# Kernel tuning notes

Measured on AMD Instinct MI355X. Metric: run time of the kernel, lower is better.

Reference implementation:

```python
import jax, jax.numpy as jnp
import numpy as np
from jax import lax

DIM = 1024
HEADS = 16
KERNEL = 7
STRIDE = 4
EPS = 1e-5


def setup_inputs() -> dict:
    key = jax.random.key(0)
    ks = jax.random.split(key, 4)
    B, N = 2, 4096
    w_scale = 0.02
    return {
        "x": jax.random.normal(ks[0], (B, N, DIM), dtype=jnp.float32),
        "ln_w": jnp.ones((DIM,), jnp.float32),
        "ln_b": jnp.zeros((DIM,), jnp.float32),
        "Wk": jax.random.normal(ks[1], (DIM, DIM, KERNEL), dtype=jnp.float32) * w_scale,
        "Wv": jax.random.normal(ks[2], (DIM, DIM, KERNEL), dtype=jnp.float32) * w_scale,
        "Wq": jax.random.normal(ks[3], (DIM, DIM, KERNEL), dtype=jnp.float32) * w_scale,
    }


def _conv1d(x_bnd, w):
    # x: (B, N, D) -> conv over sequence dim with 'same' padding; w: (out_ch, in_ch, K)
    x_cn = jnp.transpose(x_bnd, (0, 2, 1))  # (B, D, N)
    pad = KERNEL // 2
    y = lax.conv_general_dilated(
        x_cn, w, window_strides=(1,), padding=[(pad, pad)],
        dimension_numbers=("NCH", "OIH", "NCH"))
    return jnp.transpose(y, (0, 2, 1))  # (B, N, D)


def reference(x, ln_w, ln_b, Wk, Wv, Wq):
    B, N, D = x.shape
    hd = D // HEADS
    # LayerNorm (biased variance, as in torch)
    mu = jnp.mean(x, axis=-1, keepdims=True)
    var = jnp.mean(jnp.square(x - mu), axis=-1, keepdims=True)
    x_n = (x - mu) / jnp.sqrt(var + EPS) * ln_w + ln_b

    K = _conv1d(x_n, Wk)                 # (B, N, D)
    V = _conv1d(x_n, Wv)                 # (B, N, D)
    Q = _conv1d(x_n, Wq)[:, ::STRIDE]    # (B, M, D) windowed queries
    M = Q.shape[1]

    Qh = Q.reshape(B, M, HEADS, hd).transpose(0, 2, 1, 3)  # (B, H, M, hd)
    Kh = K.reshape(B, N, HEADS, hd).transpose(0, 2, 1, 3)  # (B, H, N, hd)
    Vh = V.reshape(B, N, HEADS, hd).transpose(0, 2, 1, 3)  # (B, H, N, hd)

    scale = jnp.sqrt(jnp.asarray(hd, x.dtype))
    scores = jnp.einsum("bhmd,bhnd->bhmn", Qh, Kh) / scale  # (B, H, M, N)
    attn = jax.nn.softmax(scores, axis=-1)
    out = jnp.einsum("bhmn,bhnd->bhmd", attn, Vh)           # (B, H, M, hd)
    out = out.transpose(0, 2, 1, 3).reshape(B, M, D)
    return out + Q
```

## Files before the change

kernel.cpp:

```cpp
#include <hip/hip_runtime.h>

typedef __attribute__((ext_vector_type(4))) float f32x4;
typedef __attribute__((ext_vector_type(16))) float f32x16;
typedef __attribute__((ext_vector_type(8))) short short8;
typedef __attribute__((ext_vector_type(4))) unsigned short u16x4;
typedef __attribute__((ext_vector_type(8))) unsigned short u16x8;

#define AS1 __attribute__((address_space(1)))
#define AS3 __attribute__((address_space(3)))

__device__ __forceinline__ unsigned short f2bf(float f) {
  unsigned u = __float_as_uint(f);
  return (unsigned short)((u + 0x7FFFu + ((u >> 16) & 1u)) >> 16);
}
__device__ __forceinline__ unsigned short f2bf_fast(float f) {
  return (unsigned short)((__float_as_uint(f) + 0x8000u) >> 16);
}

__global__ __launch_bounds__(256) void ln_kernel(
    const float* __restrict__ x, const float* __restrict__ lw,
    const float* __restrict__ lb, unsigned short* __restrict__ xpad) {
  __shared__ float red[8];
  int row = blockIdx.x;
  int b = row >> 12, n = row & 4095;
  const float* xr = x + (size_t)row * 1024;
  int c = threadIdx.x * 4;
  f32x4 v = *(const f32x4*)(xr + c);
  float s = v[0] + v[1] + v[2] + v[3];
  float sq = v[0]*v[0] + v[1]*v[1] + v[2]*v[2] + v[3]*v[3];
#pragma unroll
  for (int off = 32; off; off >>= 1) {
    s  += __shfl_xor(s, off, 64);
    sq += __shfl_xor(sq, off, 64);
  }
  int w = threadIdx.x >> 6;
  if ((threadIdx.x & 63) == 0) { red[w*2] = s; red[w*2+1] = sq; }
  __syncthreads();
  float S  = red[0]+red[2]+red[4]+red[6];
  float SQ = red[1]+red[3]+red[5]+red[7];
  float mean = S * (1.0f/1024.0f);
  float var  = SQ * (1.0f/1024.0f) - mean*mean;
  float rstd = rsqrtf(var + 1e-5f);
  f32x4 wv = *(const f32x4*)(lw + c);
  f32x4 bv = *(const f32x4*)(lb + c);
  u16x4 o;
#pragma unroll
  for (int r = 0; r < 4; ++r) o[r] = f2bf((v[r]-mean)*rstd*wv[r] + bv[r]);
  *(u16x4*)(xpad + (((size_t)(b*4102 + n + 3)) << 10) + c) = o;
}

__global__ __launch_bounds__(256) void repack_kernel(
    const float* __restrict__ Wk, const float* __restrict__ Wv,
    const float* __restrict__ Wq, unsigned short* __restrict__ Wt) {
  __shared__ unsigned short t[7168];
  const float* W = (blockIdx.y == 0) ? Wk : (blockIdx.y == 1) ? Wv : Wq;
  int o = blockIdx.x;
  const float* row = W + (size_t)o * 7168;
  unsigned short* orow = Wt + ((size_t)(blockIdx.y * 1024 + o)) * 7168;
#pragma unroll
  for (int p = 0; p < 7; ++p) {
    int idx = p*1024 + threadIdx.x*4;
    f32x4 v = *(const f32x4*)(row + idx);
#pragma unroll
    for (int e = 0; e < 4; ++e) {
      unsigned j = idx + e;
      unsigned i = (j * 149797u) >> 20;
      unsigned k = j - i*7;
      t[k*1024 + i] = f2bf(v[e]);
    }
  }
  __syncthreads();
#pragma unroll
  for (int p = 0; p < 7; ++p) {
    int idx = p*1024 + threadIdx.x*4;
    *(u16x4*)(orow + idx) = *(const u16x4*)(t + idx);
  }
}

__global__ __launch_bounds__(256, 4) void conv3(
    const unsigned short* __restrict__ Apad,
    const unsigned short* __restrict__ Wt,
    unsigned short* __restrict__ Ksg, unsigned short* __restrict__ Vsg,
    unsigned short* __restrict__ Qsg, float* __restrict__ Qf) {
  __shared__ unsigned short As[128*64];
  __shared__ unsigned short Bs[128*64];
  const int g = blockIdx.x;
  const int tid = threadIdx.x;
  const int w = tid >> 6, l = tid & 63;

  int mode, nt, rt;
  if (g < 1024) {
    int xcol = ((g & 7) << 1) | ((g >> 3) & 1);
    mode = (xcol < 8) ? 0 : 1;
    nt = xcol; rt = g >> 4;
  } else {
    int gq = g - 1024;
    mode = 2; nt = 16 + (gq & 7); rt = gq >> 3;
  }
  const int n0 = nt << 7;
  const int r0 = rt << 7;

  const int lrow = l >> 3;
  const int cs = (l & 7) ^ lrow;
  size_t abase0, astep, bbase0;
  {
    int r = r0 + (w << 5) + lrow;
    int bb, nn;
    if (mode == 2) { bb = r >> 10; nn = (r & 1023) << 2; astep = 8 * 4096; }
    else           { bb = r >> 12; nn = r & 4095;        astep = 8 * 1024; }
    abase0 = (((size_t)(bb*4102 + nn)) << 10) + cs*8;
    int nc = n0 + (w << 5) + lrow;
    bbase0 = (size_t)nc * 7168 + cs*8;
  }

  f32x16 acc[2][2] = {};
  const int wm = (w >> 1) << 6, wn = (w & 1) << 6;
  const int l31 = l & 31, lh = l >> 5, l7 = l & 7;

  for (int k0 = 0; k0 < 7168; k0 += 64) {
    __syncthreads();
#pragma unroll
    for (int t = 0; t < 4; ++t) {
      __builtin_amdgcn_global_load_lds((const AS1 void*)(Apad + abase0 + (size_t)t*astep + k0),
                                       (AS3 void*)(As + (((w << 2) + t) << 9)), 16, 0, 0);
      __builtin_amdgcn_global_load_lds((const AS1 void*)(Wt + bbase0 + (size_t)t*(8*7168) + k0),
                                       (AS3 void*)(Bs + (((w << 2) + t) << 9)), 16, 0, 0);
    }
    __syncthreads();
#pragma unroll
    for (int s2 = 0; s2 < 2; ++s2) {
      short8 af[2][2], bf[2][2];
#pragma unroll
      for (int i = 0; i < 2; ++i)
#pragma unroll
        for (int hs = 0; hs < 2; ++hs) {
          int s = (s2 << 1) | hs;
          int ch = (((s << 1) | lh) ^ l7) << 3;
          af[i][hs] = *(const short8*)(As + (wm + (i<<5) + l31)*64 + ch);
          bf[i][hs] = *(const short8*)(Bs + (wn + (i<<5) + l31)*64 + ch);
        }
#pragma unroll
      for (int hs = 0; hs < 2; ++hs)
#pragma unroll
        for (int i = 0; i < 2; ++i)
#pragma unroll
          for (int j = 0; j < 2; ++j)
            acc[i][j] = __builtin_amdgcn_mfma_f32_32x32x16_bf16(af[i][hs], bf[j][hs], acc[i][j], 0, 0, 0);
    }
  }

  if (mode == 0) {
#pragma unroll
    for (int i = 0; i < 2; ++i) {
      int rgb = r0 + wm + (i<<5);
      int b = rgb >> 12, nbase = rgb & 4095;
#pragma unroll
      for (int j = 0; j < 2; ++j) {
        int cg = n0 + wn + (j<<5) + l31;
        int h = cg >> 6, kd = (cg >> 5) & 1;
        size_t base = ((size_t)(((b*16 + h)*2 + kd)) << 12) * 32 + (size_t)(cg & 31);
#pragma unroll
        for (int r = 0; r < 16; ++r) {
          int nb = nbase + (r & 3) + ((r >> 2) << 3) + (lh << 2);
          Ksg[base + ((size_t)nb << 5)] = f2bf(acc[i][j][r]);
        }
      }
    }
  } else if (mode == 1) {
#pragma unroll
    for (int i = 0; i < 2; ++i) {
      int rgb = r0 + wm + (i<<5);
      int b = rgb >> 12, nbase = rgb & 4095;
      int nc = nbase >> 5;
#pragma unroll
      for (int j = 0; j < 2; ++j) {
        int c = n0 + wn + (j<<5) + l31 - 1024;
        int h = c >> 6, d = c & 63;
        size_t rowbase = ((size_t)((b*16 + h)*128 + nc) * 64 + d) << 5;
#pragma unroll
        for (int g2 = 0; g2 < 4; ++g2) {
          u16x4 pv;
#pragma unroll
          for (int e = 0; e < 4; ++e) pv[e] = f2bf(acc[i][j][g2*4 + e]);
          *(u16x4*)(Vsg + rowbase + (g2 << 3) + (lh << 2)) = pv;
        }
      }
    }
  } else {
#pragma unroll
    for (int i = 0; i < 2; ++i) {
      int rqb = r0 + wm + (i<<5);
#pragma unroll
      for (int j = 0; j < 2; ++j) {
        int cg = (n0 - 2048) + wn + (j<<5) + l31;
        int h = cg >> 6, kd = (cg >> 5) & 1, d32 = cg & 31;
#pragma unroll
        for (int r = 0; r < 16; ++r) {
          int rq = rqb + (r & 3) + ((r >> 2) << 3) + (lh << 2);
          int b = rq >> 10, m = rq & 1023;
          float vv = acc[i][j][r];
          Qsg[(((size_t)((b*16 + h)*2 + kd) * 1024 + m) << 5) + d32] = f2bf(vv);
          Qf[((size_t)rq << 10) + cg] = vv;
        }
      }
    }
  }
}

__global__ __launch_bounds__(256) void attn_kernel(
    const unsigned short* __restrict__ Ksg, const unsigned short* __restrict__ Vsg,
    const unsigned short* __restrict__ Qsg, const float* __restrict__ Qf,
    float* __restrict__ out) {
  __shared__ unsigned short Ks[8192];
  __shared__ unsigned short Vs[8192];
  __shared__ unsigned short Qs[4096];
  __shared__ unsigned short Ps[8704];
  const int tid = threadIdx.x, w = tid >> 6, l = tid & 63;
  const int g = blockIdx.x;
  const int bh = (g & 7) + (((g >> 3) & 3) << 3);
  const int qt = g >> 5;
  const int b = bh >> 4, h = bh & 15;
  const int m0 = qt << 6;
  const int quad = l >> 4, lc = l & 15, l3 = l & 3;
  const float C = 0.18033688011112042f;
  const int lsw = (l & 60) | ((l ^ (l >> 2)) & 3);

  const unsigned short* KgT = Ksg + ((size_t)bh << 18);
  const unsigned short* VgT = Vsg + ((size_t)bh << 18);
  const unsigned short* QgT = Qsg + ((size_t)bh << 16);

#pragma unroll
  for (int p = 0; p < 2; ++p) {
    int t = w*2 + p;
    int kd = t >> 2, ml = (t & 3) << 4;
    __builtin_amdgcn_global_load_lds(
        (const AS1 void*)(QgT + ((size_t)((kd << 10) + m0 + ml) << 5) + lsw*8),
        (AS3 void*)(Qs + (t << 9)), 16, 0, 0);
  }

  float l_run = 0.f;
  f32x4 oacc[4] = {};
  unsigned short* Pw = Ps + w*2176;

  for (int it = 0; it < 32; ++it) {
    int n0 = it << 7;
    __syncthreads();
#pragma unroll
    for (int p = 0; p < 4; ++p) {
      int t = (w << 2) + p;
      __builtin_amdgcn_global_load_lds(
          (const AS1 void*)(KgT + ((size_t)(((t >> 3) << 12) + n0 + ((t & 7) << 4)) << 5) + lsw*8),
          (AS3 void*)(Ks + (t << 9)), 16, 0, 0);
      __builtin_amdgcn_global_load_lds(
          (const AS1 void*)(VgT + ((size_t)((((n0 >> 5) + (t >> 2)) << 6) + ((t & 3) << 4)) << 5) + lsw*8),
          (AS3 void*)(Vs + (t << 9)), 16, 0, 0);
    }
    __syncthreads();

    const int ch = (quad ^ l3) << 3;
    short8 ak[8][2];
#pragma unroll
    for (int k = 0; k < 2; ++k)
#pragma unroll
      for (int ni = 0; ni < 8; ++ni)
        ak[ni][k] = *(const short8*)(Ks + (k << 12) + ((ni<<4) + lc)*32 + ch);

    f32x4 sv[8] = {};
#pragma unroll
    for (int k = 0; k < 2; ++k) {
      short8 bq = *(const short8*)(Qs + (k << 11) + ((w<<4) + lc)*32 + ch);
#pragma unroll
      for (int ni = 0; ni < 8; ++ni)
        sv[ni] = __builtin_amdgcn_mfma_f32_16x16x32_bf16(ak[ni][k], bq, sv[ni], 0, 0, 0);
    }

    float su = 0.f;
#pragma unroll
    for (int ni = 0; ni < 8; ++ni) {
      u16x4 pv;
#pragma unroll
      for (int rr = 0; rr < 4; ++rr) {
        float pp = __builtin_amdgcn_exp2f(sv[ni][rr] * C);
        su += pp;
        pv[rr] = f2bf_fast(pp);
      }
      *(u16x4*)(Pw + lc*136 + (ni<<4) + (quad<<2)) = pv;
    }
    su += __shfl_xor(su, 16, 64);
    su += __shfl_xor(su, 32, 64);
    l_run += su;

#pragma unroll
    for (int kn = 0; kn < 4; ++kn) {
      short8 bp = *(const short8*)(Pw + lc*136 + (kn<<5) + (quad<<3));
#pragma unroll
      for (int dt = 0; dt < 4; ++dt) {
        short8 av = *(const short8*)(Vs + (kn << 11) + ((dt<<4) + lc)*32 + ch);
        oacc[dt] = __builtin_amdgcn_mfma_f32_16x16x32_bf16(av, bp, oacc[dt], 0, 0, 0);
      }
    }
  }

  float invl = 1.0f / l_run;
  int m = m0 + (w<<4) + lc;
#pragma unroll
  for (int dt = 0; dt < 4; ++dt) {
    int d = (dt<<4) + (quad<<2);
    size_t off = (((size_t)(b << 10) + m) << 10) + (h << 6) + d;
    f32x4 qv = *(const f32x4*)(Qf + off);
    f32x4 ov;
#pragma unroll
    for (int rr = 0; rr < 4; ++rr) ov[rr] = oacc[dt][rr]*invl + qv[rr];
    *(f32x4*)(out + off) = ov;
  }
}

extern "C" void kernel_launch(void* const* d_in, const int* in_sizes, int n_in,
                              void* d_out, int out_size, void* d_ws, size_t ws_size,
                              hipStream_t stream) {
  const float* x  = (const float*)d_in[0];
  const float* lw = (const float*)d_in[1];
  const float* lb = (const float*)d_in[2];
  const float* Wk = (const float*)d_in[3];
  const float* Wv = (const float*)d_in[4];
  const float* Wq = (const float*)d_in[5];
  float* out = (float*)d_out;

  char* ws = (char*)d_ws;
  size_t off = 0;
  unsigned short* xpad = (unsigned short*)(ws + off); off += (size_t)2*4102*1024*2;
  unsigned short* Wt   = (unsigned short*)(ws + off); off += (size_t)3072*7168*2;
  unsigned short* Ksg  = (unsigned short*)(ws + off); off += (size_t)32*2*4096*32*2;
  unsigned short* Vsg  = (unsigned short*)(ws + off); off += (size_t)32*128*64*32*2;
  unsigned short* Qsg  = (unsigned short*)(ws + off); off += (size_t)32*2*1024*32*2;
  float*          Qf   = (float*)(ws + off);          off += (size_t)2048*1024*4;

  for (int b = 0; b < 2; ++b) {
    hipMemsetAsync(xpad + (size_t)b*4102*1024, 0, 3*1024*2, stream);
    hipMemsetAsync(xpad + ((size_t)b*4102 + 4099)*1024, 0, 3*1024*2, stream);
  }
  ln_kernel<<<dim3(8192), dim3(256), 0, stream>>>(x, lw, lb, xpad);
  repack_kernel<<<dim3(1024, 3), dim3(256), 0, stream>>>(Wk, Wv, Wq, Wt);
  conv3<<<dim3(1152), dim3(256), 0, stream>>>(xpad, Wt, Ksg, Vsg, Qsg, Qf);
  attn_kernel<<<dim3(512), dim3(256), 0, stream>>>(Ksg, Vsg, Qsg, Qf, out);
}
```

Measured before the change: 581.4 us.

## Rewrite conv GEMM as 256x256 double-buffered kernel with split-K Q tail

```diff
diff --git a/kernel.cpp b/kernel.cpp
--- a/kernel.cpp
+++ b/kernel.cpp
@@ -1,10 +1,8 @@
 #include <hip/hip_runtime.h>
 
 typedef __attribute__((ext_vector_type(4))) float f32x4;
-typedef __attribute__((ext_vector_type(16))) float f32x16;
 typedef __attribute__((ext_vector_type(8))) short short8;
 typedef __attribute__((ext_vector_type(4))) unsigned short u16x4;
-typedef __attribute__((ext_vector_type(8))) unsigned short u16x8;
 
 #define AS1 __attribute__((address_space(1)))
 #define AS3 __attribute__((address_space(3)))
@@ -77,134 +75,231 @@
   }
 }
 
-__global__ __launch_bounds__(256, 4) void conv3(
+__global__ __launch_bounds__(512, 2) void conv256(
     const unsigned short* __restrict__ Apad,
     const unsigned short* __restrict__ Wt,
     unsigned short* __restrict__ Ksg, unsigned short* __restrict__ Vsg,
-    unsigned short* __restrict__ Qsg, float* __restrict__ Qf) {
-  __shared__ unsigned short As[128*64];
-  __shared__ unsigned short Bs[128*64];
-  const int g = blockIdx.x;
+    float* __restrict__ Qf) {
+  __shared__ unsigned short As[2][2][8192];
+  __shared__ unsigned short Bs[2][2][8192];
+
   const int tid = threadIdx.x;
   const int w = tid >> 6, l = tid & 63;
-
-  int mode, nt, rt;
-  if (g < 1024) {
-    int xcol = ((g & 7) << 1) | ((g >> 3) & 1);
-    mode = (xcol < 8) ? 0 : 1;
-    nt = xcol; rt = g >> 4;
-  } else {
-    int gq = g - 1024;
-    mode = 2; nt = 16 + (gq & 7); rt = gq >> 3;
-  }
-  const int n0 = nt << 7;
-  const int r0 = rt << 7;
-
-  const int lrow = l >> 3;
-  const int cs = (l & 7) ^ lrow;
-  size_t abase0, astep, bbase0;
-  {
-    int r = r0 + (w << 5) + lrow;
-    int bb, nn;
-    if (mode == 2) { bb = r >> 10; nn = (r & 1023) << 2; astep = 8 * 4096; }
-    else           { bb = r >> 12; nn = r & 4095;        astep = 8 * 1024; }
-    abase0 = (((size_t)(bb*4102 + nn)) << 10) + cs*8;
-    int nc = n0 + (w << 5) + lrow;
-    bbase0 = (size_t)nc * 7168 + cs*8;
-  }
-
-  f32x16 acc[2][2] = {};
-  const int wm = (w >> 1) << 6, wn = (w & 1) << 6;
-  const int l31 = l & 31, lh = l >> 5, l7 = l & 7;
-
-  for (int k0 = 0; k0 < 7168; k0 += 64) {
-    __syncthreads();
-#pragma unroll
-    for (int t = 0; t < 4; ++t) {
-      __builtin_amdgcn_global_load_lds((const AS1 void*)(Apad + abase0 + (size_t)t*astep + k0),
-                                       (AS3 void*)(As + (((w << 2) + t) << 9)), 16, 0, 0);
-      __builtin_amdgcn_global_load_lds((const AS1 void*)(Wt + bbase0 + (size_t)t*(8*7168) + k0),
-                                       (AS3 void*)(Bs + (((w << 2) + t) << 9)), 16, 0, 0);
-    }
-    __syncthreads();
-#pragma unroll
-    for (int s2 = 0; s2 < 2; ++s2) {
-      short8 af[2][2], bf[2][2];
-#pragma unroll
-      for (int i = 0; i < 2; ++i)
-#pragma unroll
-        for (int hs = 0; hs < 2; ++hs) {
-          int s = (s2 << 1) | hs;
-          int ch = (((s << 1) | lh) ^ l7) << 3;
-          af[i][hs] = *(const short8*)(As + (wm + (i<<5) + l31)*64 + ch);
-          bf[i][hs] = *(const short8*)(Bs + (wn + (i<<5) + l31)*64 + ch);
-        }
-#pragma unroll
-      for (int hs = 0; hs < 2; ++hs)
-#pragma unroll
-        for (int i = 0; i < 2; ++i)
-#pragma unroll
-          for (int j = 0; j < 2; ++j)
-            acc[i][j] = __builtin_amdgcn_mfma_f32_32x32x16_bf16(af[i][hs], bf[j][hs], acc[i][j], 0, 0, 0);
-    }
-  }
-
-  if (mode == 0) {
-#pragma unroll
-    for (int i = 0; i < 2; ++i) {
-      int rgb = r0 + wm + (i<<5);
-      int b = rgb >> 12, nbase = rgb & 4095;
-#pragma unroll
-      for (int j = 0; j < 2; ++j) {
-        int cg = n0 + wn + (j<<5) + l31;
-        int h = cg >> 6, kd = (cg >> 5) & 1;
-        size_t base = ((size_t)(((b*16 + h)*2 + kd)) << 12) * 32 + (size_t)(cg & 31);
-#pragma unroll
-        for (int r = 0; r < 16; ++r) {
-          int nb = nbase + (r & 3) + ((r >> 2) << 3) + (lh << 2);
-          Ksg[base + ((size_t)nb << 5)] = f2bf(acc[i][j][r]);
+  const int wm = w >> 2, wn = w & 3;
+  const int l15 = l & 15, lh4 = l >> 4, l7 = l & 7;
+  const int chA = ((l7 & 4) | (lh4 ^ (l7 & 3))) << 3;
+  const int wOff = w << 9;
+  const int bid = blockIdx.x;
+  const int ct = bid & 7, rt = bid >> 3;
+
+  unsigned aOff[2][2], bOff[2][2];
+#pragma unroll
+  for (int i = 0; i < 2; ++i) {
+    const int idx = i * 512 + tid;
+    const int r = idx >> 3;
+    const int clog8 = (((idx & 7) ^ (r & 7)) << 3);
+#pragma unroll
+    for (int hh = 0; hh < 2; ++hh) {
+      const int rg = (rt << 8) + (hh << 7) + r;
+      aOff[hh][i] = ((unsigned)((rg >> 12) * 4102 + (rg & 4095)) << 10) + clog8;
+      const int cg = (ct << 8) + (hh << 7) + r;
+      bOff[hh][i] = (unsigned)cg * 7168u + clog8;
+    }
+  }
+
+  unsigned aRd[4], bRd[2];
+#pragma unroll
+  for (int fm = 0; fm < 4; ++fm)
+    aRd[fm] = (unsigned)(((wm << 6) + (fm << 4) + l15) << 6) + chA;
+#pragma unroll
+  for (int fn = 0; fn < 2; ++fn)
+    bRd[fn] = (unsigned)(((wn << 5) + (fn << 4) + l15) << 6) + chA;
+
+  f32x4 acc[2][2][4][2] = {};
+  short8 af[4][2], bfr[2][2];
+
+#define STGA(BUF, HALF, T) do { \
+    __builtin_amdgcn_global_load_lds((const AS1 void*)(Apad + aOff[HALF][0] + ((unsigned)(T) << 6)), (AS3 void*)&As[BUF][HALF][wOff], 16, 0, 0); \
+    __builtin_amdgcn_global_load_lds((const AS1 void*)(Apad + aOff[HALF][1] + ((unsigned)(T) << 6)), (AS3 void*)&As[BUF][HALF][4096 + wOff], 16, 0, 0); \
+  } while (0)
+#define STGB(BUF, HALF, T) do { \
+    __builtin_amdgcn_global_load_lds((const AS1 void*)(Wt + bOff[HALF][0] + ((unsigned)(T) << 6)), (AS3 void*)&Bs[BUF][HALF][wOff], 16, 0, 0); \
+    __builtin_amdgcn_global_load_lds((const AS1 void*)(Wt + bOff[HALF][1] + ((unsigned)(T) << 6)), (AS3 void*)&Bs[BUF][HALF][4096 + wOff], 16, 0, 0); \
+  } while (0)
+#define LDA(BUF, MQ) do { \
+    _Pragma("unroll") for (int fm = 0; fm < 4; ++fm) { \
+      af[fm][0] = *(const short8*)&As[BUF][MQ][aRd[fm]]; \
+      af[fm][1] = *(const short8*)&As[BUF][MQ][aRd[fm] ^ 32u]; } \
+  } while (0)
+#define LDB(BUF, NQ) do { \
+    _Pragma("unroll") for (int fn = 0; fn < 2; ++fn) { \
+      bfr[fn][0] = *(const short8*)&Bs[BUF][NQ][bRd[fn]]; \
+      bfr[fn][1] = *(const short8*)&Bs[BUF][NQ][bRd[fn] ^ 32u]; } \
+  } while (0)
+#define MM(MQ, NQ) do { \
+    _Pragma("unroll") for (int ks = 0; ks < 2; ++ks) \
+    _Pragma("unroll") for (int fm = 0; fm < 4; ++fm) \
+    _Pragma("unroll") for (int fn = 0; fn < 2; ++fn) \
+      acc[MQ][NQ][fm][fn] = __builtin_amdgcn_mfma_f32_16x16x32_bf16(af[fm][ks], bfr[fn][ks], acc[MQ][NQ][fm][fn], 0, 0, 0); \
+  } while (0)
+#define BAR __builtin_amdgcn_s_barrier()
+#define LGKM0 asm volatile("s_waitcnt lgkmcnt(0)" ::: "memory")
+#define VM6 asm volatile("s_waitcnt vmcnt(6)" ::: "memory")
+#define VM0 asm volatile("s_waitcnt vmcnt(0)" ::: "memory")
+#define P1 __builtin_amdgcn_s_setprio(1)
+#define P0 __builtin_amdgcn_s_setprio(0)
+
+#define RUN_GEMM(NIT) do { \
+    STGA(0, 0, 0); STGB(0, 0, 0); STGA(0, 1, 0); STGB(0, 1, 0); \
+    STGA(1, 0, 1); STGB(1, 1, 1); STGA(1, 1, 1); \
+    VM6; BAR; \
+    for (int I = 0; I < (NIT) - 1; ++I) { \
+      const int t0 = I * 2; \
+      LDA(0, 0); LDB(0, 0); STGB(1, 0, t0 + 1); \
+      BAR; LGKM0; P1; MM(0, 0); P0; BAR; \
+      LDB(0, 1);            STGA(0, 0, t0 + 2); \
+      BAR; LGKM0; P1; MM(0, 1); P0; BAR; \
+      LDA(0, 1);            STGB(0, 1, t0 + 2); \
+      BAR; LGKM0; P1; MM(1, 1); P0; BAR; \
+      LDB(0, 0);            STGA(0, 1, t0 + 2); \
+      BAR; LGKM0; P1; MM(1, 0); P0; VM6; BAR; \
+      LDA(1, 0); LDB(1, 0); STGB(0, 0, t0 + 2); \
+      BAR; LGKM0; P1; MM(0, 0); P0; BAR; \
+      LDB(1, 1);            STGA(1, 0, t0 + 3); \
+      BAR; LGKM0; P1; MM(0, 1); P0; BAR; \
+      LDA(1, 1);            STGB(1, 1, t0 + 3); \
+      BAR; LGKM0; P1; MM(1, 1); P0; BAR; \
+      LDB(1, 0);            STGA(1, 1, t0 + 3); \
+      BAR; LGKM0; P1; MM(1, 0); P0; VM6; BAR; \
+    } \
+    { const int t0 = ((NIT) - 1) * 2; \
+      LDA(0, 0); LDB(0, 0); STGB(1, 0, t0 + 1); \
+      BAR; LGKM0; P1; MM(0, 0); P0; BAR; \
+      LDB(0, 1); BAR; LGKM0; P1; MM(0, 1); P0; BAR; \
+      LDA(0, 1); BAR; LGKM0; P1; MM(1, 1); P0; BAR; \
+      LDB(0, 0); BAR; LGKM0; P1; MM(1, 0); P0; VM0; BAR; \
+      LDA(1, 0); LDB(1, 0); BAR; LGKM0; P1; MM(0, 0); P0; BAR; \
+      LDB(1, 1); BAR; LGKM0; P1; MM(0, 1); P0; BAR; \
+      LDA(1, 1); BAR; LGKM0; P1; MM(1, 1); P0; BAR; \
+      LDB(1, 0); BAR; LGKM0; P1; MM(1, 0); P0; BAR; \
+    } \
+  } while (0)
+
+  RUN_GEMM(56);
+
+  if (ct < 4) {
+#pragma unroll
+    for (int mq = 0; mq < 2; ++mq)
+#pragma unroll
+      for (int nq = 0; nq < 2; ++nq) {
+        const int h = (ct << 2) + (nq << 1) + (wn >> 1);
+        const int kd = wn & 1;
+#pragma unroll
+        for (int fm = 0; fm < 4; ++fm) {
+          const int rbase = (rt << 8) + (mq << 7) + (wm << 6) + (fm << 4) + (lh4 << 2);
+          const int b = rbase >> 12, n0 = rbase & 4095;
+          const size_t base = ((((size_t)((b * 16 + h) * 2 + kd)) << 12) + n0) << 5;
+#pragma unroll
+          for (int fn = 0; fn < 2; ++fn) {
+            const int d32 = (fn << 4) + l15;
+#pragma unroll
+            for (int rr = 0; rr < 4; ++rr)
+              Ksg[base + ((size_t)rr << 5) + d32] = f2bf(acc[mq][nq][fm][fn][rr]);
+          }
         }
       }
-    }
-  } else if (mode == 1) {
-#pragma unroll
-    for (int i = 0; i < 2; ++i) {
-      int rgb = r0 + wm + (i<<5);
-      int b = rgb >> 12, nbase = rgb & 4095;
-      int nc = nbase >> 5;
-#pragma unroll
-      for (int j = 0; j < 2; ++j) {
-        int c = n0 + wn + (j<<5) + l31 - 1024;
-        int h = c >> 6, d = c & 63;
-        size_t rowbase = ((size_t)((b*16 + h)*128 + nc) * 64 + d) << 5;
-#pragma unroll
-        for (int g2 = 0; g2 < 4; ++g2) {
-          u16x4 pv;
-#pragma unroll
-          for (int e = 0; e < 4; ++e) pv[e] = f2bf(acc[i][j][g2*4 + e]);
-          *(u16x4*)(Vsg + rowbase + (g2 << 3) + (lh << 2)) = pv;
+  } else {
+#pragma unroll
+    for (int mq = 0; mq < 2; ++mq)
+#pragma unroll
+      for (int nq = 0; nq < 2; ++nq) {
+        const int h = ((ct - 4) << 2) + (nq << 1) + (wn >> 1);
+        const int dhi = (wn & 1) << 5;
+#pragma unroll
+        for (int fm = 0; fm < 4; ++fm) {
+          const int rbase = (rt << 8) + (mq << 7) + (wm << 6) + (fm << 4) + (lh4 << 2);
+          const int b = rbase >> 12, n = rbase & 4095;
+#pragma unroll
+          for (int fn = 0; fn < 2; ++fn) {
+            const int d = dhi + (fn << 4) + l15;
+            const size_t rowbase =
+                ((((((size_t)(b * 16 + h)) << 7) + (n >> 5)) << 6) + d) * 32 + (n & 31);
+            u16x4 pv;
+#pragma unroll
+            for (int rr = 0; rr < 4; ++rr) pv[rr] = f2bf(acc[mq][nq][fm][fn][rr]);
+            *(u16x4*)(Vsg + rowbase) = pv;
+          }
         }
       }
-    }
-  } else {
-#pragma unroll
-    for (int i = 0; i < 2; ++i) {
-      int rqb = r0 + wm + (i<<5);
-#pragma unroll
-      for (int j = 0; j < 2; ++j) {
-        int cg = (n0 - 2048) + wn + (j<<5) + l31;
-        int h = cg >> 6, kd = (cg >> 5) & 1, d32 = cg & 31;
-#pragma unroll
-        for (int r = 0; r < 16; ++r) {
-          int rq = rqb + (r & 3) + ((r >> 2) << 3) + (lh << 2);
-          int b = rq >> 10, m = rq & 1023;
-          float vv = acc[i][j][r];
-          Qsg[(((size_t)((b*16 + h)*2 + kd) * 1024 + m) << 5) + d32] = f2bf(vv);
-          Qf[((size_t)rq << 10) + cg] = vv;
+  }
+
+  const int qct = bid & 3, qrt = (bid >> 2) & 7, kc = bid >> 5;
+  const unsigned kbase = (unsigned)kc * 896u;
+#pragma unroll
+  for (int i = 0; i < 2; ++i) {
+    const int idx = i * 512 + tid;
+    const int r = idx >> 3;
+    const int clog8 = (((idx & 7) ^ (r & 7)) << 3);
+#pragma unroll
+    for (int hh = 0; hh < 2; ++hh) {
+      const int rg = (qrt << 8) + (hh << 7) + r;
+      aOff[hh][i] = ((unsigned)((rg >> 10) * 4102 + ((rg & 1023) << 2)) << 10) + clog8 + kbase;
+      const int cg = 2048 + (qct << 8) + (hh << 7) + r;
+      bOff[hh][i] = (unsigned)cg * 7168u + clog8 + kbase;
+    }
+  }
+#pragma unroll
+  for (int mq = 0; mq < 2; ++mq)
+#pragma unroll
+    for (int nq = 0; nq < 2; ++nq)
+#pragma unroll
+      for (int fm = 0; fm < 4; ++fm)
+#pragma unroll
+        for (int fn = 0; fn < 2; ++fn)
+          acc[mq][nq][fm][fn] = (f32x4){0.f, 0.f, 0.f, 0.f};
+
+  RUN_GEMM(7);
+
+#pragma unroll
+  for (int mq = 0; mq < 2; ++mq)
+#pragma unroll
+    for (int nq = 0; nq < 2; ++nq)
+#pragma unroll
+      for (int fm = 0; fm < 4; ++fm) {
+        const int rq = (qrt << 8) + (mq << 7) + (wm << 6) + (fm << 4) + (lh4 << 2);
+#pragma unroll
+        for (int fn = 0; fn < 2; ++fn) {
+          const int cq = (qct << 8) + (nq << 7) + (wn << 5) + (fn << 4) + l15;
+#pragma unroll
+          for (int rr = 0; rr < 4; ++rr)
+            atomicAdd(Qf + (((size_t)(rq + rr)) << 10) + cq, acc[mq][nq][fm][fn][rr]);
         }
       }
-    }
-  }
+#undef STGA
+#undef STGB
+#undef LDA
+#undef LDB
+#undef MM
+#undef BAR
+#undef LGKM0
+#undef VM6
+#undef VM0
+#undef P1
+#undef P0
+#undef RUN_GEMM
+}
+
+__global__ __launch_bounds__(256) void qfinal(
+    const float* __restrict__ Qf, unsigned short* __restrict__ Qsg) {
+  const int rq = blockIdx.x;
+  const int b = rq >> 10, m = rq & 1023;
+  const int c = threadIdx.x << 2;
+  f32x4 v = *(const f32x4*)(Qf + ((size_t)rq << 10) + c);
+  const int h = c >> 6, kd = (c >> 5) & 1, d32 = c & 31;
+  u16x4 o;
+#pragma unroll
+  for (int e = 0; e < 4; ++e) o[e] = f2bf(v[e]);
+  *(u16x4*)(Qsg + ((((size_t)((b * 16 + h) * 2 + kd)) << 10) + m) * 32 + d32) = o;
 }
 
 __global__ __launch_bounds__(256) void attn_kernel(
@@ -335,12 +430,14 @@
   unsigned short* Qsg  = (unsigned short*)(ws + off); off += (size_t)32*2*1024*32*2;
   float*          Qf   = (float*)(ws + off);          off += (size_t)2048*1024*4;
 
+  hipMemsetAsync(Qf, 0, (size_t)2048*1024*4, stream);
   for (int b = 0; b < 2; ++b) {
     hipMemsetAsync(xpad + (size_t)b*4102*1024, 0, 3*1024*2, stream);
     hipMemsetAsync(xpad + ((size_t)b*4102 + 4099)*1024, 0, 3*1024*2, stream);
   }
   ln_kernel<<<dim3(8192), dim3(256), 0, stream>>>(x, lw, lb, xpad);
   repack_kernel<<<dim3(1024, 3), dim3(256), 0, stream>>>(Wk, Wv, Wq, Wt);
-  conv3<<<dim3(1152), dim3(256), 0, stream>>>(xpad, Wt, Ksg, Vsg, Qsg, Qf);
+  conv256<<<dim3(256), dim3(512), 0, stream>>>(xpad, Wt, Ksg, Vsg, Qf);
+  qfinal<<<dim3(2048), dim3(256), 0, stream>>>(Qf, Qsg);
   attn_kernel<<<dim3(512), dim3(256), 0, stream>>>(Ksg, Vsg, Qsg, Qf, out);
 }
```

Measured after the change: 535.8 us. 7.8% less time.
